# Optimization experiments

Measured on AMD Instinct MI355X. Metric: run time of the kernel, lower is better.

## Reference

```python
import jax, jax.numpy as jnp
import numpy as np

NP, NO, E, IN_DIM, D = 100000, 200000, 500000, 512, 256
EPS = 1e-12  # torch F.normalize default eps


def setup_inputs() -> dict:
    key = jax.random.key(0)
    ks = jax.random.split(key, 12)
    return {
        "feat_prefix": jax.random.normal(ks[0], (NP, IN_DIM), jnp.float32),
        "feat_other": jax.random.normal(ks[1], (NO, IN_DIM), jnp.float32),
        "src": jax.random.randint(ks[2], (E,), 0, NP),
        "dst": jax.random.randint(ks[3], (E,), 0, NO),
        "Wm_p": jax.random.normal(ks[4], (IN_DIM, D), jnp.float32) * 0.02,
        "bm_p": jax.random.normal(ks[5], (D,), jnp.float32) * 0.02,
        "Wm_o": jax.random.normal(ks[6], (IN_DIM, D), jnp.float32) * 0.02,
        "bm_o": jax.random.normal(ks[7], (D,), jnp.float32) * 0.02,
        "W": jax.random.normal(ks[8], (D, D), jnp.float32) * 0.02,
        "bW": jax.random.normal(ks[9], (D,), jnp.float32) * 0.02,
        "a_w": jax.random.normal(ks[10], (2 * D,), jnp.float32) * 0.02,
        "a_b": jax.random.normal(ks[11], (1,), jnp.float32) * 0.02,
    }


def _l2norm(x):
    n = jnp.linalg.norm(x, axis=-1, keepdims=True)
    return x / jnp.maximum(n, EPS)


def reference(feat_prefix, feat_other, src, dst,
              Wm_p, bm_p, Wm_o, bm_o, W, bW, a_w, a_b):
    # FeatureMappingLayer: per-ntype Linear + ReLU
    hp = jax.nn.relu(feat_prefix @ Wm_p + bm_p)   # [NP, D]
    ho = jax.nn.relu(feat_other @ Wm_o + bm_o)    # [NO, D]
    d = hp.shape[1]
    n_prefix = hp.shape[0]

    # GAT-style score: a([W h_src ; W h_dst]) -- project at node level,
    # decompose the concat-linear into two per-node dot products, then gather.
    hp_proj = hp @ W + bW                         # [NP, D]
    ho_proj = ho @ W + bW                         # [NO, D]
    s_src = hp_proj @ a_w[:d]                     # [NP]
    s_dst = ho_proj @ a_w[d:]                     # [NO]
    e = s_src[src] + s_dst[dst] + a_b[0]          # [E] per-edge scores

    # Segment softmax over source (Prefix) node
    m = jax.ops.segment_max(e, src, num_segments=n_prefix)
    m = jnp.where(jnp.isfinite(m), m, 0.0)        # empty segments -> 0
    ex = jnp.exp(e - m[src])
    denom = jax.ops.segment_sum(ex, src, num_segments=n_prefix)
    alpha = ex / denom[src]                       # [E]

    # Scatter-weighted sum of mapped (pre-W) dst features into Prefix nodes
    agg = jax.ops.segment_sum(alpha[:, None] * ho[dst], src,
                              num_segments=n_prefix)  # [NP, D]

    return (_l2norm(agg), _l2norm(ho))
```

## Files before the change

### kernel.cpp

```cpp
#include <hip/hip_runtime.h>
#include <math.h>

#define IN_DIM 512
#define DD 256

typedef _Float16 half8_t __attribute__((ext_vector_type(8)));
typedef __attribute__((ext_vector_type(4))) float f32x4_t;

__global__ __launch_bounds__(256) void prep_w2(const float* __restrict__ W,
                                               const float* __restrict__ a_w,
                                               float* __restrict__ w2) {
  int row = (blockIdx.x * 256 + threadIdx.x) >> 6;
  int lane = threadIdx.x & 63;
  if (row >= DD) return;
  float4 wv = *reinterpret_cast<const float4*>(&W[(size_t)row * DD + lane * 4]);
  float4 av = *reinterpret_cast<const float4*>(&a_w[DD + lane * 4]);
  float s = wv.x * av.x + wv.y * av.y + wv.z * av.z + wv.w * av.w;
#pragma unroll
  for (int d = 32; d; d >>= 1) s += __shfl_xor(s, d, 64);
  if (lane == 0) w2[row] = s;
}

__global__ void bconv_kernel(const float* __restrict__ Wm, _Float16* __restrict__ Bh) {
  int i = blockIdx.x * 256 + threadIdx.x;
  int k = i >> 8, col = i & 255;
  int kc16 = k >> 5, kr = k & 31;
  int lane = ((kr >> 3) << 4) | (col & 15);
  int nf = col >> 4;
  int off = (((((kc16 << 4) + nf) << 6) + lane) << 3) + (kr & 7);
  Bh[off] = (_Float16)Wm[i];
}

__device__ __forceinline__ half8_t cvt8(const float4& a, const float4& b) {
  half8_t h;
  h[0] = (_Float16)a.x; h[1] = (_Float16)a.y; h[2] = (_Float16)a.z; h[3] = (_Float16)a.w;
  h[4] = (_Float16)b.x; h[5] = (_Float16)b.y; h[6] = (_Float16)b.z; h[7] = (_Float16)b.w;
  return h;
}

__device__ __forceinline__ void gload16(const void* g, void* l) {
  __builtin_amdgcn_global_load_lds(
      (const __attribute__((address_space(1))) void*)g,
      (__attribute__((address_space(3))) void*)l, 16, 0, 0);
}

__global__ __launch_bounds__(256, 2) void map_gemm_mfma(
    const float* __restrict__ X, const _Float16* __restrict__ Bh,
    const float* __restrict__ bm, const float* __restrict__ w2,
    float* __restrict__ Yn, _Float16* __restrict__ Y16,
    float* __restrict__ wnorm, int M) {
  __shared__ _Float16 Bs[3][8192];
  const int t = threadIdx.x;
  const int wv = t >> 6;
  const int l = t & 63;
  const int c = l & 15;
  const int g = l >> 4;
  const int row0 = blockIdx.x * 128 + wv * 32;

  int arow0 = row0 + c;       if (arow0 >= M) arow0 = M - 1;
  int arow1 = row0 + 16 + c;  if (arow1 >= M) arow1 = M - 1;
  const float* xrow0 = X + (size_t)arow0 * IN_DIM;
  const float* xrow1 = X + (size_t)arow1 * IN_DIM;

  f32x4_t acc[2][16];
#pragma unroll
  for (int rf = 0; rf < 2; ++rf)
#pragma unroll
    for (int n = 0; n < 16; ++n) acc[rf][n] = (f32x4_t){0.f, 0.f, 0.f, 0.f};

  const char* bbytes = reinterpret_cast<const char*>(Bh);
  const int lane16 = l * 16;

  float4 a0[2][2], a1[2][2];
#pragma unroll
  for (int j = 0; j < 4; ++j)
    gload16(bbytes + ((wv << 2) + j) * 1024 + lane16,
            (char*)&Bs[0][0] + ((wv << 2) + j) * 1024);
  a0[0][0] = *reinterpret_cast<const float4*>(xrow0 + g * 8);
  a0[0][1] = *reinterpret_cast<const float4*>(xrow0 + g * 8 + 4);
  a0[1][0] = *reinterpret_cast<const float4*>(xrow1 + g * 8);
  a0[1][1] = *reinterpret_cast<const float4*>(xrow1 + g * 8 + 4);
  asm volatile("" ::: "memory");
#pragma unroll
  for (int j = 0; j < 4; ++j)
    gload16(bbytes + 16384 + ((wv << 2) + j) * 1024 + lane16,
            (char*)&Bs[1][0] + ((wv << 2) + j) * 1024);
  a1[0][0] = *reinterpret_cast<const float4*>(xrow0 + 32 + g * 8);
  a1[0][1] = *reinterpret_cast<const float4*>(xrow0 + 32 + g * 8 + 4);
  a1[1][0] = *reinterpret_cast<const float4*>(xrow1 + 32 + g * 8);
  a1[1][1] = *reinterpret_cast<const float4*>(xrow1 + 32 + g * 8 + 4);

#pragma unroll
  for (int kc = 0; kc < 16; ++kc) {
    if (kc < 15) {
      asm volatile("s_waitcnt vmcnt(8)" ::: "memory");
    } else {
      asm volatile("s_waitcnt vmcnt(0)" ::: "memory");
    }
    __builtin_amdgcn_s_barrier();
    asm volatile("" ::: "memory");
    __builtin_amdgcn_sched_barrier(0);

    half8_t ah0, ah1;
    if ((kc & 1) == 0) {
      ah0 = cvt8(a0[0][0], a0[0][1]);
      ah1 = cvt8(a0[1][0], a0[1][1]);
    } else {
      ah0 = cvt8(a1[0][0], a1[0][1]);
      ah1 = cvt8(a1[1][0], a1[1][1]);
    }

    if (kc < 14) {
      const char* gb = bbytes + (kc + 2) * 16384;
      char* lb = (char*)&Bs[(kc + 2) % 3][0];
#pragma unroll
      for (int j = 0; j < 4; ++j)
        gload16(gb + ((wv << 2) + j) * 1024 + lane16, lb + ((wv << 2) + j) * 1024);
      const float* xp0 = xrow0 + (kc + 2) * 32 + g * 8;
      const float* xp1 = xrow1 + (kc + 2) * 32 + g * 8;
      if ((kc & 1) == 0) {
        a0[0][0] = *reinterpret_cast<const float4*>(xp0);
        a0[0][1] = *reinterpret_cast<const float4*>(xp0 + 4);
        a0[1][0] = *reinterpret_cast<const float4*>(xp1);
        a0[1][1] = *reinterpret_cast<const float4*>(xp1 + 4);
      } else {
        a1[0][0] = *reinterpret_cast<const float4*>(xp0);
        a1[0][1] = *reinterpret_cast<const float4*>(xp0 + 4);
        a1[1][0] = *reinterpret_cast<const float4*>(xp1);
        a1[1][1] = *reinterpret_cast<const float4*>(xp1 + 4);
      }
    }

    const _Float16* bp = &Bs[kc % 3][0];
    __builtin_amdgcn_s_setprio(1);
#pragma unroll
    for (int n = 0; n < 16; ++n) {
      half8_t bh = *reinterpret_cast<const half8_t*>(&bp[n * 512 + l * 8]);
      acc[0][n] = __builtin_amdgcn_mfma_f32_16x16x32_f16(ah0, bh, acc[0][n], 0, 0, 0);
      acc[1][n] = __builtin_amdgcn_mfma_f32_16x16x32_f16(ah1, bh, acc[1][n], 0, 0, 0);
    }
    __builtin_amdgcn_s_setprio(0);
  }

#pragma unroll
  for (int rf = 0; rf < 2; ++rf) {
    float ssq[4] = {0.f, 0.f, 0.f, 0.f}, dtq[4] = {0.f, 0.f, 0.f, 0.f};
#pragma unroll
    for (int n = 0; n < 16; ++n) {
      float bvn = bm[n * 16 + c];
      float wvn = w2[n * 16 + c];
#pragma unroll
      for (int q = 0; q < 4; ++q) {
        float v = acc[rf][n][q] + bvn;
        v = v > 0.f ? v : 0.f;
        acc[rf][n][q] = v;
        ssq[q] = fmaf(v, v, ssq[q]);
        dtq[q] = fmaf(v, wvn, dtq[q]);
      }
    }
#pragma unroll
    for (int q = 0; q < 4; ++q) {
#pragma unroll
      for (int d = 1; d < 16; d <<= 1) {
        ssq[q] += __shfl_xor(ssq[q], d, 16);
        dtq[q] += __shfl_xor(dtq[q], d, 16);
      }
    }
    float inv[4];
#pragma unroll
    for (int q = 0; q < 4; ++q) {
      float nr = sqrtf(ssq[q]);
      inv[q] = 1.f / fmaxf(nr, 1e-12f);
      int r = row0 + rf * 16 + g * 4 + q;
      if (c == 0 && r < M) wnorm[r] = expf(dtq[q]) * nr;
    }
#pragma unroll
    for (int q = 0; q < 4; ++q) {
      int r = row0 + rf * 16 + g * 4 + q;
      if (r < M) {
#pragma unroll
        for (int n = 0; n < 16; ++n) {
          float v = acc[rf][n][q] * inv[q];
          Yn[(size_t)r * DD + n * 16 + c] = v;
          Y16[(size_t)r * DD + n * 16 + c] = (_Float16)v;
        }
      }
    }
  }
}

__global__ void hist_kernel(const int* __restrict__ src, int* __restrict__ deg, int E) {
  int i = blockIdx.x * blockDim.x + threadIdx.x;
  if (i < E) atomicAdd(&deg[src[i]], 1);
}

__global__ __launch_bounds__(256) void scan_part(const int* __restrict__ deg,
                                                 int* __restrict__ bsum, int NP) {
  __shared__ int s[256];
  int t = threadIdx.x, b = blockIdx.x;
  int i0 = (b * 256 + t) * 2;
  int v0 = (i0 < NP) ? deg[i0] : 0;
  int v1 = (i0 + 1 < NP) ? deg[i0 + 1] : 0;
  s[t] = v0 + v1;
  __syncthreads();
  for (int off = 128; off; off >>= 1) {
    if (t < off) s[t] += s[t + off];
    __syncthreads();
  }
  if (t == 0) bsum[b] = s[0];
}

__global__ __launch_bounds__(256) void scan_fin2(const int* __restrict__ deg,
                                                 const int* __restrict__ bsum,
                                                 int* __restrict__ rowptr,
                                                 int* __restrict__ cursor, int NP) {
  __shared__ int s[256];
  __shared__ int base_s;
  int t = threadIdx.x, b = blockIdx.x;
  int v = (t < b) ? bsum[t] : 0;
  s[t] = v;
  __syncthreads();
  for (int off = 128; off; off >>= 1) {
    if (t < off) s[t] += s[t + off];
    __syncthreads();
  }
  if (t == 0) base_s = s[0];
  __syncthreads();
  int base0 = base_s;
  __syncthreads();
  int i0 = (b * 256 + t) * 2;
  int v0 = (i0 < NP) ? deg[i0] : 0;
  int v1 = (i0 + 1 < NP) ? deg[i0 + 1] : 0;
  int local = v0 + v1;
  s[t] = local;
  __syncthreads();
  for (int off = 1; off < 256; off <<= 1) {
    int u = (t >= off) ? s[t - off] : 0;
    __syncthreads();
    s[t] += u;
    __syncthreads();
  }
  int myb = base0 + s[t] - local;
  if (i0 < NP) { rowptr[i0] = myb; cursor[i0] = myb; }
  if (i0 + 1 < NP) { rowptr[i0 + 1] = myb + v0; cursor[i0 + 1] = myb + v0; }
  if (b == gridDim.x - 1 && t == 255) rowptr[NP] = base0 + s[255];
}

__global__ void fill_kernel(const int* __restrict__ src, const int* __restrict__ dst,
                            int* __restrict__ cursor, int* __restrict__ ebuf, int E) {
  int i = blockIdx.x * blockDim.x + threadIdx.x;
  if (i < E) {
    int pos = atomicAdd(&cursor[src[i]], 1);
    ebuf[pos] = dst[i];
  }
}

__global__ __launch_bounds__(256) void agg_kernel(const int* __restrict__ rowptr,
                                                  const int* __restrict__ ebuf,
                                                  const float* __restrict__ wnorm,
                                                  const _Float16* __restrict__ hon16,
                                                  float* __restrict__ agg, int NP) {
  long gid = (long)blockIdx.x * blockDim.x + threadIdx.x;
  int wid = (int)(gid >> 6);
  int lane = threadIdx.x & 63;
  int sg = lane >> 4;
  int li = lane & 15;
  int p = wid * 4 + sg;
  if (p >= NP) return;
  int beg = rowptr[p], end = rowptr[p + 1];
  float acc[16];
#pragma unroll
  for (int k = 0; k < 16; ++k) acc[k] = 0.f;
  if (beg < end) {
    int d = ebuf[beg];
    float w = wnorm[d];
    const half8_t* rp = reinterpret_cast<const half8_t*>(&hon16[(size_t)d * DD + li * 16]);
    half8_t v0 = rp[0], v1 = rp[1];
    for (int j = beg + 1; j <= end; ++j) {
      half8_t n0, n1;
      float wn_ = 0.f;
      bool have = (j < end);
      if (have) {
        int dn = ebuf[j];
        wn_ = wnorm[dn];
        const half8_t* np_ = reinterpret_cast<const half8_t*>(&hon16[(size_t)dn * DD + li * 16]);
        n0 = np_[0]; n1 = np_[1];
      }
#pragma unroll
      for (int k = 0; k < 8; ++k) {
        acc[k] = fmaf(w, (float)v0[k], acc[k]);
        acc[8 + k] = fmaf(w, (float)v1[k], acc[8 + k]);
      }
      if (have) { w = wn_; v0 = n0; v1 = n1; }
    }
  }
  float ss = 0.f;
#pragma unroll
  for (int k = 0; k < 16; ++k) ss = fmaf(acc[k], acc[k], ss);
#pragma unroll
  for (int d2 = 8; d2 > 0; d2 >>= 1) ss += __shfl_xor(ss, d2, 16);
  float inv = 1.0f / fmaxf(sqrtf(ss), 1e-12f);
  float* op = &agg[(size_t)p * DD + li * 16];
#pragma unroll
  for (int k = 0; k < 4; ++k) {
    float4 o = {acc[k * 4] * inv, acc[k * 4 + 1] * inv,
                acc[k * 4 + 2] * inv, acc[k * 4 + 3] * inv};
    *reinterpret_cast<float4*>(op + k * 4) = o;
  }
}

extern "C" void kernel_launch(void* const* d_in, const int* in_sizes, int n_in,
                              void* d_out, int out_size, void* d_ws, size_t ws_size,
                              hipStream_t stream) {
  const float* feat_other = (const float*)d_in[1];
  const int* src = (const int*)d_in[2];
  const int* dst = (const int*)d_in[3];
  const float* Wm_o = (const float*)d_in[6];
  const float* bm_o = (const float*)d_in[7];
  const float* W = (const float*)d_in[8];
  const float* a_w = (const float*)d_in[10];

  const int NP = in_sizes[0] / IN_DIM;
  const int NO = in_sizes[1] / IN_DIM;
  const int E = in_sizes[2];

  float* out = (float*)d_out;
  float* agg_out = out;
  float* ho_out = out + (size_t)NP * DD;

  float* ws = (float*)d_ws;
  float* wnorm = ws;
  float* w2 = wnorm + NO;
  int* deg = (int*)(w2 + 256);
  int* rowptr = deg + NP;
  int* cursor = rowptr + NP + 1;
  int* bsum = cursor + NP;
  int* ebuf = bsum + 256;
  size_t foff = (size_t)NO + 256 + NP + (NP + 1) + NP + 256 + E;
  foff = (foff + 3) & ~(size_t)3;
  _Float16* Bh = (_Float16*)(ws + foff);
  _Float16* Y16 = Bh + (size_t)IN_DIM * DD;

  hipMemsetAsync(deg, 0, (size_t)NP * sizeof(int), stream);

  prep_w2<<<64, 256, 0, stream>>>(W, a_w, w2);
  bconv_kernel<<<(IN_DIM * DD) / 256, 256, 0, stream>>>(Wm_o, Bh);

  map_gemm_mfma<<<(NO + 127) / 128, 256, 0, stream>>>(
      feat_other, Bh, bm_o, w2, ho_out, Y16, wnorm, NO);

  hist_kernel<<<(E + 255) / 256, 256, 0, stream>>>(src, deg, E);
  scan_part<<<256, 256, 0, stream>>>(deg, bsum, NP);
  scan_fin2<<<256, 256, 0, stream>>>(deg, bsum, rowptr, cursor, NP);
  fill_kernel<<<(E + 255) / 256, 256, 0, stream>>>(src, dst, cursor, ebuf, E);

  agg_kernel<<<(NP + 15) / 16, 256, 0, stream>>>(
      rowptr, ebuf, wnorm, Y16, agg_out, NP);
}
```

Measured before the change: 332.1 us.

## Shrink GEMM tile to 32 rows with column-split waves and double buffering

Restructures the mapping GEMM so each block handles 32 rows instead of 128. The four waves split as 2 row halves × 2 column halves, each wave keeping 8 accumulator tiles instead of 32. The LDS ring buffer drops from three stages to two, and launch bounds go up to 4 blocks per CU, aiming for more occupancy and more blocks to spread across CUs. Row norms and attention dot products are now reduced across the two column-half waves through shared memory. In exchange, every block loads the full weight matrix for only 32 rows, so weight traffic from L2 rises about 4x, and there is less prefetch depth plus an extra barrier per k-step.

Result: slower. 404.8 us (+21.9%).

```diff
diff --git a/kernel.cpp b/kernel.cpp
--- a/kernel.cpp
+++ b/kernel.cpp
@@ -44,146 +44,141 @@
       (__attribute__((address_space(3))) void*)l, 16, 0, 0);
 }
 
-__global__ __launch_bounds__(256, 2) void map_gemm_mfma(
+__global__ __launch_bounds__(256, 4) void map_gemm_mfma(
     const float* __restrict__ X, const _Float16* __restrict__ Bh,
     const float* __restrict__ bm, const float* __restrict__ w2,
     float* __restrict__ Yn, _Float16* __restrict__ Y16,
     float* __restrict__ wnorm, int M) {
-  __shared__ _Float16 Bs[3][8192];
+  __shared__ _Float16 Bs[2][8192];
   const int t = threadIdx.x;
-  const int wv = t >> 6;
+  const int w = t >> 6;
   const int l = t & 63;
   const int c = l & 15;
   const int g = l >> 4;
-  const int row0 = blockIdx.x * 128 + wv * 32;
-
-  int arow0 = row0 + c;       if (arow0 >= M) arow0 = M - 1;
-  int arow1 = row0 + 16 + c;  if (arow1 >= M) arow1 = M - 1;
-  const float* xrow0 = X + (size_t)arow0 * IN_DIM;
-  const float* xrow1 = X + (size_t)arow1 * IN_DIM;
-
-  f32x4_t acc[2][16];
-#pragma unroll
-  for (int rf = 0; rf < 2; ++rf)
-#pragma unroll
-    for (int n = 0; n < 16; ++n) acc[rf][n] = (f32x4_t){0.f, 0.f, 0.f, 0.f};
+  const int rh = w & 1;
+  const int ch = w >> 1;
+  const int row0 = blockIdx.x * 32 + rh * 16;
+
+  int arow = row0 + c;
+  if (arow >= M) arow = M - 1;
+  const float* xrow = X + (size_t)arow * IN_DIM;
+
+  f32x4_t acc[8];
+#pragma unroll
+  for (int n = 0; n < 8; ++n) acc[n] = (f32x4_t){0.f, 0.f, 0.f, 0.f};
 
   const char* bbytes = reinterpret_cast<const char*>(Bh);
-  const int lane16 = l * 16;
-
-  float4 a0[2][2], a1[2][2];
+  const int soff = (w << 12) + (l << 4);
+
+  float4 a0[2], a1[2];
+
 #pragma unroll
   for (int j = 0; j < 4; ++j)
-    gload16(bbytes + ((wv << 2) + j) * 1024 + lane16,
-            (char*)&Bs[0][0] + ((wv << 2) + j) * 1024);
-  a0[0][0] = *reinterpret_cast<const float4*>(xrow0 + g * 8);
-  a0[0][1] = *reinterpret_cast<const float4*>(xrow0 + g * 8 + 4);
-  a0[1][0] = *reinterpret_cast<const float4*>(xrow1 + g * 8);
-  a0[1][1] = *reinterpret_cast<const float4*>(xrow1 + g * 8 + 4);
+    gload16(bbytes + soff + j * 1024, (char*)&Bs[0][0] + soff + j * 1024);
+  a0[0] = *reinterpret_cast<const float4*>(xrow + g * 8);
+  a0[1] = *reinterpret_cast<const float4*>(xrow + g * 8 + 4);
+  asm volatile("s_waitcnt vmcnt(0)" ::: "memory");
+  __builtin_amdgcn_s_barrier();
   asm volatile("" ::: "memory");
-#pragma unroll
-  for (int j = 0; j < 4; ++j)
-    gload16(bbytes + 16384 + ((wv << 2) + j) * 1024 + lane16,
-            (char*)&Bs[1][0] + ((wv << 2) + j) * 1024);
-  a1[0][0] = *reinterpret_cast<const float4*>(xrow0 + 32 + g * 8);
-  a1[0][1] = *reinterpret_cast<const float4*>(xrow0 + 32 + g * 8 + 4);
-  a1[1][0] = *reinterpret_cast<const float4*>(xrow1 + 32 + g * 8);
-  a1[1][1] = *reinterpret_cast<const float4*>(xrow1 + 32 + g * 8 + 4);
+  __builtin_amdgcn_sched_barrier(0);
 
 #pragma unroll
   for (int kc = 0; kc < 16; ++kc) {
+    const int cur = kc & 1;
+    half8_t ah = (cur == 0) ? cvt8(a0[0], a0[1]) : cvt8(a1[0], a1[1]);
+
     if (kc < 15) {
-      asm volatile("s_waitcnt vmcnt(8)" ::: "memory");
-    } else {
+      const char* gb = bbytes + (kc + 1) * 16384;
+      char* lb = (char*)&Bs[cur ^ 1][0];
+#pragma unroll
+      for (int j = 0; j < 4; ++j)
+        gload16(gb + soff + j * 1024, lb + soff + j * 1024);
+      const float* xp = xrow + (kc + 1) * 32 + g * 8;
+      if (cur == 0) {
+        a1[0] = *reinterpret_cast<const float4*>(xp);
+        a1[1] = *reinterpret_cast<const float4*>(xp + 4);
+      } else {
+        a0[0] = *reinterpret_cast<const float4*>(xp);
+        a0[1] = *reinterpret_cast<const float4*>(xp + 4);
+      }
+    }
+
+    const _Float16* bp = &Bs[cur][0];
+    __builtin_amdgcn_s_setprio(1);
+#pragma unroll
+    for (int n = 0; n < 8; ++n) {
+      half8_t bh = *reinterpret_cast<const half8_t*>(&bp[((ch << 3) + n) * 512 + l * 8]);
+      acc[n] = __builtin_amdgcn_mfma_f32_16x16x32_f16(ah, bh, acc[n], 0, 0, 0);
+    }
+    __builtin_amdgcn_s_setprio(0);
+
+    if (kc < 15) {
       asm volatile("s_waitcnt vmcnt(0)" ::: "memory");
-    }
-    __builtin_amdgcn_s_barrier();
-    asm volatile("" ::: "memory");
-    __builtin_amdgcn_sched_barrier(0);
-
-    half8_t ah0, ah1;
-    if ((kc & 1) == 0) {
-      ah0 = cvt8(a0[0][0], a0[0][1]);
-      ah1 = cvt8(a0[1][0], a0[1][1]);
-    } else {
-      ah0 = cvt8(a1[0][0], a1[0][1]);
-      ah1 = cvt8(a1[1][0], a1[1][1]);
-    }
-
-    if (kc < 14) {
-      const char* gb = bbytes + (kc + 2) * 16384;
-      char* lb = (char*)&Bs[(kc + 2) % 3][0];
-#pragma unroll
-      for (int j = 0; j < 4; ++j)
-        gload16(gb + ((wv << 2) + j) * 1024 + lane16, lb + ((wv << 2) + j) * 1024);
-      const float* xp0 = xrow0 + (kc + 2) * 32 + g * 8;
-      const float* xp1 = xrow1 + (kc + 2) * 32 + g * 8;
-      if ((kc & 1) == 0) {
-        a0[0][0] = *reinterpret_cast<const float4*>(xp0);
-        a0[0][1] = *reinterpret_cast<const float4*>(xp0 + 4);
-        a0[1][0] = *reinterpret_cast<const float4*>(xp1);
-        a0[1][1] = *reinterpret_cast<const float4*>(xp1 + 4);
-      } else {
-        a1[0][0] = *reinterpret_cast<const float4*>(xp0);
-        a1[0][1] = *reinterpret_cast<const float4*>(xp0 + 4);
-        a1[1][0] = *reinterpret_cast<const float4*>(xp1);
-        a1[1][1] = *reinterpret_cast<const float4*>(xp1 + 4);
-      }
-    }
-
-    const _Float16* bp = &Bs[kc % 3][0];
-    __builtin_amdgcn_s_setprio(1);
-#pragma unroll
-    for (int n = 0; n < 16; ++n) {
-      half8_t bh = *reinterpret_cast<const half8_t*>(&bp[n * 512 + l * 8]);
-      acc[0][n] = __builtin_amdgcn_mfma_f32_16x16x32_f16(ah0, bh, acc[0][n], 0, 0, 0);
-      acc[1][n] = __builtin_amdgcn_mfma_f32_16x16x32_f16(ah1, bh, acc[1][n], 0, 0, 0);
-    }
-    __builtin_amdgcn_s_setprio(0);
-  }
-
-#pragma unroll
-  for (int rf = 0; rf < 2; ++rf) {
-    float ssq[4] = {0.f, 0.f, 0.f, 0.f}, dtq[4] = {0.f, 0.f, 0.f, 0.f};
-#pragma unroll
-    for (int n = 0; n < 16; ++n) {
-      float bvn = bm[n * 16 + c];
-      float wvn = w2[n * 16 + c];
-#pragma unroll
-      for (int q = 0; q < 4; ++q) {
-        float v = acc[rf][n][q] + bvn;
-        v = v > 0.f ? v : 0.f;
-        acc[rf][n][q] = v;
-        ssq[q] = fmaf(v, v, ssq[q]);
-        dtq[q] = fmaf(v, wvn, dtq[q]);
-      }
-    }
+      __builtin_amdgcn_s_barrier();
+      asm volatile("" ::: "memory");
+      __builtin_amdgcn_sched_barrier(0);
+    }
+  }
+
+  float ssq[4] = {0.f, 0.f, 0.f, 0.f}, dtq[4] = {0.f, 0.f, 0.f, 0.f};
+#pragma unroll
+  for (int n = 0; n < 8; ++n) {
+    int col = (ch << 7) + (n << 4) + c;
+    float bvn = bm[col];
+    float wvn = w2[col];
 #pragma unroll
     for (int q = 0; q < 4; ++q) {
-#pragma unroll
-      for (int d = 1; d < 16; d <<= 1) {
-        ssq[q] += __shfl_xor(ssq[q], d, 16);
-        dtq[q] += __shfl_xor(dtq[q], d, 16);
-      }
-    }
-    float inv[4];
+      float v = acc[n][q] + bvn;
+      v = v > 0.f ? v : 0.f;
+      acc[n][q] = v;
+      ssq[q] = fmaf(v, v, ssq[q]);
+      dtq[q] = fmaf(v, wvn, dtq[q]);
+    }
+  }
+#pragma unroll
+  for (int q = 0; q < 4; ++q) {
+#pragma unroll
+    for (int d = 1; d < 16; d <<= 1) {
+      ssq[q] += __shfl_xor(ssq[q], d, 16);
+      dtq[q] += __shfl_xor(dtq[q], d, 16);
+    }
+  }
+  float* red = reinterpret_cast<float*>(&Bs[0][0]);
+  __syncthreads();
+  if (c == 0) {
 #pragma unroll
     for (int q = 0; q < 4; ++q) {
-      float nr = sqrtf(ssq[q]);
-      inv[q] = 1.f / fmaxf(nr, 1e-12f);
-      int r = row0 + rf * 16 + g * 4 + q;
-      if (c == 0 && r < M) wnorm[r] = expf(dtq[q]) * nr;
-    }
-#pragma unroll
-    for (int q = 0; q < 4; ++q) {
-      int r = row0 + rf * 16 + g * 4 + q;
-      if (r < M) {
-#pragma unroll
-        for (int n = 0; n < 16; ++n) {
-          float v = acc[rf][n][q] * inv[q];
-          Yn[(size_t)r * DD + n * 16 + c] = v;
-          Y16[(size_t)r * DD + n * 16 + c] = (_Float16)v;
-        }
+      int rr = (g << 2) + q;
+      red[((((rh << 1) + ch) << 4) + rr) * 2 + 0] = ssq[q];
+      red[((((rh << 1) + ch) << 4) + rr) * 2 + 1] = dtq[q];
+    }
+  }
+  __syncthreads();
+  float inv[4];
+#pragma unroll
+  for (int q = 0; q < 4; ++q) {
+    int rr = (g << 2) + q;
+    float ss = red[(((rh << 1) + 0) << 4) * 2 + rr * 2 + 0] +
+               red[(((rh << 1) + 1) << 4) * 2 + rr * 2 + 0];
+    float nr = sqrtf(ss);
+    inv[q] = 1.f / fmaxf(nr, 1e-12f);
+    int r = row0 + rr;
+    if (c == 0 && ch == 0 && r < M) {
+      float dt = red[(((rh << 1) + 0) << 4) * 2 + rr * 2 + 1] +
+                 red[(((rh << 1) + 1) << 4) * 2 + rr * 2 + 1];
+      wnorm[r] = expf(dt) * nr;
+    }
+  }
+#pragma unroll
+  for (int q = 0; q < 4; ++q) {
+    int r = row0 + (g << 2) + q;
+    if (r < M) {
+#pragma unroll
+      for (int n = 0; n < 8; ++n) {
+        float v = acc[n][q] * inv[q];
+        int col = (ch << 7) + (n << 4) + c;
+        Yn[(size_t)r * DD + col] = v;
+        Y16[(size_t)r * DD + col] = (_Float16)v;
       }
     }
   }
@@ -346,7 +341,7 @@
   prep_w2<<<64, 256, 0, stream>>>(W, a_w, w2);
   bconv_kernel<<<(IN_DIM * DD) / 256, 256, 0, stream>>>(Wm_o, Bh);
 
-  map_gemm_mfma<<<(NO + 127) / 128, 256, 0, stream>>>(
+  map_gemm_mfma<<<(NO + 31) / 32, 256, 0, stream>>>(
       feat_other, Bh, bm_o, w2, ho_out, Y16, wnorm, NO);
 
   hist_kernel<<<(E + 255) / 256, 256, 0, stream>>>(src, deg, E);
```
